# Performance work log

Measured on AMD Instinct MI355X. Metric: run time of the kernel, lower is better.

The kernel has to match this reference:

```python
import jax, jax.numpy as jnp
import numpy as np

# Sizes (see init_kwargs / shape_source)
N = 65536      # total points
B = 8          # batch elements
PPB = N // B   # points per batch element (8192, divisible by WS -> no padding)
D = 256        # d_model
H = 8          # nhead
DH = D // H
L = 4          # num_layers
FF = 2048      # torch TransformerEncoderLayer default dim_feedforward
RES = 128      # resolution (coordinate range / embedding table size)
BITS = 7       # ceil(log2(RES)); higher bits of morton loop are zero
WS = 128       # window_size
EPS = 1e-5     # LayerNorm eps


def setup_inputs() -> dict:
    key = jax.random.key(0)
    ks = jax.random.split(key, 16)
    s = 0.02
    batch_col = (jnp.arange(N) // PPB).astype(jnp.int32)
    xyz = jax.random.randint(ks[0], (N, 3), 0, RES, dtype=jnp.int32)
    coords = jnp.concatenate([batch_col[:, None], xyz], axis=1)
    features = jax.random.normal(ks[1], (N, D), jnp.float32)
    inp = {
        'coords': coords,
        'features': features,
        # learned positional embedding tables
        'pe_x': jax.random.normal(ks[2], (RES, D), jnp.float32) * s,
        'pe_y': jax.random.normal(ks[3], (RES, D), jnp.float32) * s,
        'pe_z': jax.random.normal(ks[4], (RES, D), jnp.float32) * s,
        'pe_s': jax.random.normal(ks[5], (RES, D), jnp.float32) * s,
        # stacked transformer encoder layer params (torch post-norm layer)
        'Wqkv': jax.random.normal(ks[6], (L, 3 * D, D), jnp.float32) * s,
        'bqkv': jnp.zeros((L, 3 * D), jnp.float32),
        'Wo': jax.random.normal(ks[7], (L, D, D), jnp.float32) * s,
        'bo': jnp.zeros((L, D), jnp.float32),
        'W1': jax.random.normal(ks[8], (L, FF, D), jnp.float32) * s,
        'b1': jnp.zeros((L, FF), jnp.float32),
        'W2': jax.random.normal(ks[9], (L, D, FF), jnp.float32) * s,
        'b2': jnp.zeros((L, D), jnp.float32),
        'g1': jnp.ones((L, D), jnp.float32),
        'be1': jnp.zeros((L, D), jnp.float32),
        'g2': jnp.ones((L, D), jnp.float32),
        'be2': jnp.zeros((L, D), jnp.float32),
    }
    return inp


def _morton_key(coords):
    # interleave bits of x,y,z (z lowest), prefix with batch index so batch order is preserved
    x, y, z = coords[:, 1], coords[:, 2], coords[:, 3]
    m = jnp.zeros_like(x)
    for i in range(BITS):
        m = m | (((x >> i) & 1) << (3 * i + 2)) \
              | (((y >> i) & 1) << (3 * i + 1)) \
              | (((z >> i) & 1) << (3 * i))
    return coords[:, 0] * (1 << (3 * BITS)) + m


def _ln(x, g, b):
    mu = jnp.mean(x, axis=-1, keepdims=True)
    var = jnp.mean(jnp.square(x - mu), axis=-1, keepdims=True)
    return (x - mu) * jax.lax.rsqrt(var + EPS) * g + b


def _encoder(x, params):
    # x: [Wn, WS, D]; torch TransformerEncoderLayer, post-norm, relu, no dropout (eval)
    scale = float(DH) ** -0.5

    def layer(h, p):
        Wqkv, bqkv, Wo, bo, W1, b1, W2, b2, g1, be1, g2, be2 = p
        Wn = h.shape[0]
        qkv = h @ Wqkv.T + bqkv                      # [Wn, WS, 3D]
        q, k, v = jnp.split(qkv, 3, axis=-1)
        q = q.reshape(Wn, WS, H, DH)
        k = k.reshape(Wn, WS, H, DH)
        v = v.reshape(Wn, WS, H, DH)
        att = jax.nn.softmax(jnp.einsum('wqhd,wkhd->whqk', q, k) * scale, axis=-1)
        o = jnp.einsum('whqk,wkhd->wqhd', att, v).reshape(Wn, WS, D) @ Wo.T + bo
        h = _ln(h + o, g1, be1)
        ff = jax.nn.relu(h @ W1.T + b1) @ W2.T + b2
        h = _ln(h + ff, g2, be2)
        return h, None

    x, _ = jax.lax.scan(layer, x, params)
    return x


def reference(coords, features, pe_x, pe_y, pe_z, pe_s,
              Wqkv, bqkv, Wo, bo, W1, b1, W2, b2, g1, be1, g2, be2):
    # 1) Morton sort (stable, batch-major)
    idx = jnp.argsort(_morton_key(coords))
    sc = coords[idx]
    sf = features[idx]
    # 2) learned positional encoding (stride = 1)
    pe = pe_x[sc[:, 1]] + pe_y[sc[:, 2]] + pe_z[sc[:, 3]] + pe_s[1]
    x = sf + pe
    # 3) window split: PPB % WS == 0, interval == 1 -> exact tiling, no padding
    x = x.reshape(-1, WS, D)                          # [Wn, WS, D]
    # 4) transformer encoder over windows
    x = _encoder(x, (Wqkv, bqkv, Wo, bo, W1, b1, W2, b2, g1, be1, g2, be2))
    # 5) gather back (all masks True -> simple reshape); output in sorted order
    return x.reshape(N, D)
```

## Files before the change

kernel.cpp:

```cpp
#include <hip/hip_runtime.h>

typedef unsigned int u32;
typedef unsigned short u16;

#define NPTS 65536
#define DMODEL 256
#define NHEAD 8
#define DHEAD 32
#define NLAYER 4
#define FFDIM 2048
#define WSIZE 128
#define LNEPS 1e-5f
#define RG 256

#define KSTR 36
#define VSTR 132
#define PSTR 132

typedef __attribute__((ext_vector_type(8))) short short8;
typedef __attribute__((ext_vector_type(4))) float floatx4;

__device__ __forceinline__ float bf2f(u16 v) {
    u32 u = ((u32)v) << 16;
    float f;
    __builtin_memcpy(&f, &u, 4);
    return f;
}
__device__ __forceinline__ u16 f2bf(float f) {
    u32 u;
    __builtin_memcpy(&u, &f, 4);
    u32 r = (u + 0x7fffu + ((u >> 16) & 1u)) >> 16;
    return (u16)r;
}

__device__ __forceinline__ void gl_lds16(const void* g, void* l) {
    __builtin_amdgcn_global_load_lds((const __attribute__((address_space(1))) u32*)g,
                                     (__attribute__((address_space(3))) u32*)l, 16, 0, 0);
}

__global__ __launch_bounds__(256) void morton_kernel(const int* __restrict__ coords,
                                                     u32* __restrict__ key, u32* __restrict__ val,
                                                     u32* __restrict__ ghist) {
    __shared__ u32 hh[256];
    int tid = threadIdx.x;
    hh[tid] = 0;
    int i = blockIdx.x * 256 + tid;
    int b = coords[4 * i + 0];
    int x = coords[4 * i + 1];
    int y = coords[4 * i + 2];
    int z = coords[4 * i + 3];
    u32 m = 0;
#pragma unroll
    for (int t = 0; t < 7; ++t) {
        m |= ((u32)((x >> t) & 1) << (3 * t + 2)) | ((u32)((y >> t) & 1) << (3 * t + 1)) |
             ((u32)((z >> t) & 1) << (3 * t));
    }
    u32 k = ((u32)b << 21) | m;
    key[i] = k;
    val[i] = (u32)i;
    __syncthreads();
    atomicAdd(&hh[k & 255u], 1u);
    __syncthreads();
    ghist[(size_t)tid * RG + blockIdx.x] = hh[tid];
}

__global__ __launch_bounds__(256) void hist_kernel(const u32* __restrict__ key, u32* __restrict__ ghist,
                                                   int shift) {
    __shared__ u32 h[256];
    int tid = threadIdx.x;
    h[tid] = 0;
    __syncthreads();
    u32 k = key[blockIdx.x * 256 + tid];
    atomicAdd(&h[(k >> shift) & 255u], 1u);
    __syncthreads();
    ghist[(size_t)tid * RG + blockIdx.x] = h[tid];
}

__global__ __launch_bounds__(256) void scan_up(u32* __restrict__ g, u32* __restrict__ aux) {
    __shared__ u32 wsum[4];
    int tid = threadIdx.x;
    int lane = tid & 63;
    int wave = tid >> 6;
    size_t base = (size_t)blockIdx.x * 1024 + (size_t)tid * 4;
    uint4 v = *(const uint4*)(g + base);
    u32 s = v.x + v.y + v.z + v.w;
    u32 inc = s;
#pragma unroll
    for (int off = 1; off < 64; off <<= 1) {
        u32 u = __shfl_up(inc, off, 64);
        if (lane >= off) inc += u;
    }
    if (lane == 63) wsum[wave] = inc;
    __syncthreads();
    u32 woff = 0;
    for (int w = 0; w < wave; ++w) woff += wsum[w];
    u32 excl = woff + inc - s;
    uint4 o;
    o.x = excl;
    o.y = excl + v.x;
    o.z = excl + v.x + v.y;
    o.w = excl + v.x + v.y + v.z;
    *(uint4*)(g + base) = o;
    if (tid == 255) aux[blockIdx.x] = woff + inc;
}

__global__ __launch_bounds__(256) void scatter_kernel(const u32* __restrict__ keyin, const u32* __restrict__ valin,
                                                      u32* __restrict__ keyout, u32* __restrict__ valout,
                                                      const u32* __restrict__ ghist, const u32* __restrict__ aux,
                                                      int shift) {
    __shared__ u32 whist[4][256];
    __shared__ u32 apre[64];
    int tid = threadIdx.x;
    int lane = tid & 63;
    int wave = tid >> 6;
    uint4 z = {0u, 0u, 0u, 0u};
    ((uint4*)&whist[0][0])[tid] = z;
    if (tid < 64) {
        u32 a = aux[tid];
        u32 inc = a;
#pragma unroll
        for (int off = 1; off < 64; off <<= 1) {
            u32 u = __shfl_up(inc, off, 64);
            if (lane >= off) inc += u;
        }
        apre[tid] = inc - a;
    }
    int gi = blockIdx.x * 256 + tid;
    u32 k = keyin[gi];
    u32 v = valin[gi];
    u32 b = (k >> shift) & 255u;
    __syncthreads();
    unsigned long long m = ~0ull;
#pragma unroll
    for (int bit = 0; bit < 8; ++bit) {
        unsigned long long bb = __ballot((int)((b >> bit) & 1u));
        m &= ((b >> bit) & 1u) ? bb : ~bb;
    }
    unsigned long long below = (lane == 0) ? 0ull : (m & ((1ull << lane) - 1ull));
    int rlane = __popcll(below);
    int cnt = __popcll(m);
    if (rlane == 0) whist[wave][b] = (u32)cnt;
    __syncthreads();
    u32 rank = (u32)rlane;
    for (int w = 0; w < wave; ++w) rank += whist[w][b];
    u32 e = b * (u32)RG + blockIdx.x;
    u32 dst = ghist[e] + apre[e >> 10] + rank;
    keyout[dst] = k;
    valout[dst] = v;
}

__global__ __launch_bounds__(256) void cvt_all_kernel(const float* __restrict__ s1, u16* __restrict__ d1, int n1,
                                                      const float* __restrict__ s2, u16* __restrict__ d2, int n2,
                                                      const float* __restrict__ s3, u16* __restrict__ d3, int n3,
                                                      const float* __restrict__ s4, u16* __restrict__ d4, int n4) {
    int i = blockIdx.x * 256 + threadIdx.x;
    if (i < n1) { d1[i] = f2bf(s1[i]); return; }
    i -= n1;
    if (i < n2) { d2[i] = f2bf(s2[i]); return; }
    i -= n2;
    if (i < n3) { d3[i] = f2bf(s3[i]); return; }
    i -= n3;
    if (i < n4) d4[i] = f2bf(s4[i]);
}

template <bool HF32>
__global__ __launch_bounds__(256) void gather_pe_kernel(const u32* __restrict__ idx, const int* __restrict__ coords,
                                                        const float* __restrict__ feat,
                                                        const float* __restrict__ pex, const float* __restrict__ pey,
                                                        const float* __restrict__ pez, const float* __restrict__ pes,
                                                        float* __restrict__ h, u16* __restrict__ xb) {
    int row = blockIdx.x * 4 + (threadIdx.x >> 6);
    int lane = threadIdx.x & 63;
    int src = (int)idx[row];
    int cx = coords[4 * src + 1];
    int cy = coords[4 * src + 2];
    int cz = coords[4 * src + 3];
    int c = lane * 4;
    float4 f = *(const float4*)(feat + (size_t)src * DMODEL + c);
    float4 px = *(const float4*)(pex + (size_t)cx * DMODEL + c);
    float4 py = *(const float4*)(pey + (size_t)cy * DMODEL + c);
    float4 pz = *(const float4*)(pez + (size_t)cz * DMODEL + c);
    float4 ps = *(const float4*)(pes + (size_t)1 * DMODEL + c);
    float4 r;
    r.x = f.x + px.x + py.x + pz.x + ps.x;
    r.y = f.y + px.y + py.y + pz.y + ps.y;
    r.z = f.z + px.z + py.z + pz.z + ps.z;
    r.w = f.w + px.w + py.w + pz.w + ps.w;
    if (HF32) *(float4*)(h + (size_t)row * DMODEL + c) = r;
    ushort4 o;
    o.x = f2bf(r.x);
    o.y = f2bf(r.y);
    o.z = f2bf(r.z);
    o.w = f2bf(r.w);
    *(ushort4*)(xb + (size_t)row * DMODEL + c) = o;
}

template <bool RELU, bool BF16OUT>
__global__ __launch_bounds__(256, 5) void gemm_bt(const u16* __restrict__ A, const u16* __restrict__ W,
                                                  const float* __restrict__ bias, void* __restrict__ Cout,
                                                  int M, int O, int K, size_t sz) {
    __shared__ __align__(16) u16 lA[2 * 128 * 32];
    __shared__ __align__(16) u16 lB[2 * 128 * 32];
    const int tid = threadIdx.x;
    const int lane = tid & 63;
    const int wave = tid >> 6;
    const int wr = wave >> 1;
    const int wc = wave & 1;
    const int quad = lane >> 4;
    const int l16 = lane & 15;
    const int kz = blockIdx.z;
    const int Kpart = K / (int)gridDim.z;
    const size_t row0 = (size_t)blockIdx.x * 128;
    const size_t col0 = (size_t)blockIdx.y * 128;
    floatx4 acc[4][4] = {};

    const int r0 = tid >> 2;
    const int sg0 = (tid & 3) ^ ((r0 >> 1) & 3);
    const u16* pA = A + (row0 + r0) * (size_t)K + (size_t)kz * Kpart + (sg0 << 3);
    const u16* pW = W + (col0 + r0) * (size_t)K + (size_t)kz * Kpart + (sg0 << 3);
    const size_t rstep = (size_t)64 * K;
    const int oA = tid * 8;

    const int nt = Kpart >> 5;
    gl_lds16(pA, lA + oA);
    gl_lds16(pA + rstep, lA + oA + 2048);
    gl_lds16(pW, lB + oA);
    gl_lds16(pW + rstep, lB + oA + 2048);
    pA += 32;
    pW += 32;

    const int sx = (quad ^ ((l16 >> 1) & 3)) << 3;
    const int rdA = (wr * 64 + l16) * 32 + sx;
    const int rdB = (wc * 64 + l16) * 32 + sx;
    int buf = 0;
    for (int t = 0; t < nt; ++t) {
        if (t + 1 < nt) {
            const int nb = (buf ^ 1) * 4096;
            gl_lds16(pA, lA + nb + oA);
            gl_lds16(pA + rstep, lA + nb + oA + 2048);
            gl_lds16(pW, lB + nb + oA);
            gl_lds16(pW + rstep, lB + nb + oA + 2048);
            pA += 32;
            pW += 32;
            asm volatile("s_waitcnt vmcnt(4)" ::: "memory");
        } else {
            asm volatile("s_waitcnt vmcnt(0)" ::: "memory");
        }
        __builtin_amdgcn_s_barrier();
        const u16* la = lA + buf * 4096 + rdA;
        const u16* lb = lB + buf * 4096 + rdB;
        short8 af[4], bf[4];
#pragma unroll
        for (int r = 0; r < 4; ++r) af[r] = *(const short8*)(la + r * 512);
#pragma unroll
        for (int c = 0; c < 4; ++c) bf[c] = *(const short8*)(lb + c * 512);
#pragma unroll
        for (int r = 0; r < 4; ++r)
#pragma unroll
            for (int c = 0; c < 4; ++c)
                acc[r][c] = __builtin_amdgcn_mfma_f32_16x16x32_bf16(af[r], bf[c], acc[r][c], 0, 0, 0);
        if (t + 1 < nt) __builtin_amdgcn_s_barrier();
        buf ^= 1;
    }

    float* Cf = (float*)Cout + (size_t)kz * sz;
#pragma unroll
    for (int r = 0; r < 4; ++r) {
#pragma unroll
        for (int c = 0; c < 4; ++c) {
            size_t col = col0 + wc * 64 + c * 16 + l16;
            float bv = (kz == 0) ? bias[col] : 0.f;
#pragma unroll
            for (int reg = 0; reg < 4; ++reg) {
                size_t row = row0 + wr * 64 + r * 16 + quad * 4 + reg;
                float v = acc[r][c][reg] + bv;
                if (RELU) v = fmaxf(v, 0.f);
                if (BF16OUT)
                    ((u16*)Cout)[row * O + col] = f2bf(v);
                else
                    Cf[row * O + col] = v;
            }
        }
    }
}

__global__ __launch_bounds__(256, 2) void gemm_w1(const u16* __restrict__ A, const u16* __restrict__ W,
                                                  const float* __restrict__ bias, u16* __restrict__ Cout,
                                                  int O, int K) {
    __shared__ __align__(16) u16 lA[2 * 128 * 32];
    __shared__ __align__(16) u16 lB[2 * 256 * 32];
    const int tid = threadIdx.x;
    const int lane = tid & 63;
    const int wave = tid >> 6;
    const int wr = wave >> 1;
    const int wc = wave & 1;
    const int quad = lane >> 4;
    const int l16 = lane & 15;
    const size_t row0 = (size_t)blockIdx.x * 128;
    const size_t col0 = (size_t)blockIdx.y * 256;
    floatx4 acc[4][8] = {};

    const int r0 = tid >> 2;
    const int sg0 = (tid & 3) ^ ((r0 >> 1) & 3);
    const u16* pA = A + (row0 + r0) * (size_t)K + (sg0 << 3);
    const u16* pW = W + (col0 + r0) * (size_t)K + (sg0 << 3);
    const size_t rstep = (size_t)64 * K;
    const int oA = tid * 8;

    const int nt = K >> 5;
    gl_lds16(pA, lA + oA);
    gl_lds16(pA + rstep, lA + oA + 2048);
    gl_lds16(pW, lB + oA);
    gl_lds16(pW + rstep, lB + oA + 2048);
    gl_lds16(pW + 2 * rstep, lB + oA + 4096);
    gl_lds16(pW + 3 * rstep, lB + oA + 6144);
    pA += 32;
    pW += 32;

    const int sx = (quad ^ ((l16 >> 1) & 3)) << 3;
    const int rdA = (wr * 64 + l16) * 32 + sx;
    const int rdB = (wc * 128 + l16) * 32 + sx;
    int buf = 0;
    for (int t = 0; t < nt; ++t) {
        if (t + 1 < nt) {
            const int na = (buf ^ 1) * 4096;
            const int nb = (buf ^ 1) * 8192;
            gl_lds16(pA, lA + na + oA);
            gl_lds16(pA + rstep, lA + na + oA + 2048);
            gl_lds16(pW, lB + nb + oA);
            gl_lds16(pW + rstep, lB + nb + oA + 2048);
            gl_lds16(pW + 2 * rstep, lB + nb + oA + 4096);
            gl_lds16(pW + 3 * rstep, lB + nb + oA + 6144);
            pA += 32;
            pW += 32;
            asm volatile("s_waitcnt vmcnt(6)" ::: "memory");
        } else {
            asm volatile("s_waitcnt vmcnt(0)" ::: "memory");
        }
        __builtin_amdgcn_s_barrier();
        const u16* la = lA + buf * 4096 + rdA;
        const u16* lb = lB + buf * 8192 + rdB;
        short8 af[4], bf[8];
#pragma unroll
        for (int r = 0; r < 4; ++r) af[r] = *(const short8*)(la + r * 512);
#pragma unroll
        for (int c = 0; c < 8; ++c) bf[c] = *(const short8*)(lb + c * 512);
#pragma unroll
        for (int r = 0; r < 4; ++r)
#pragma unroll
            for (int c = 0; c < 8; ++c)
                acc[r][c] = __builtin_amdgcn_mfma_f32_16x16x32_bf16(af[r], bf[c], acc[r][c], 0, 0, 0);
        if (t + 1 < nt) __builtin_amdgcn_s_barrier();
        buf ^= 1;
    }

#pragma unroll
    for (int r = 0; r < 4; ++r) {
#pragma unroll
        for (int c = 0; c < 8; ++c) {
            size_t col = col0 + wc * 128 + c * 16 + l16;
            float bv = bias[col];
#pragma unroll
            for (int reg = 0; reg < 4; ++reg) {
                size_t row = row0 + wr * 64 + r * 16 + quad * 4 + reg;
                float v = fmaxf(acc[r][c][reg] + bv, 0.f);
                Cout[row * O + col] = f2bf(v);
            }
        }
    }
}

__global__ __launch_bounds__(128) void attn_kernel(const u16* __restrict__ qkv, u16* __restrict__ outb) {
    const int wh = blockIdx.x;
    const int w = wh >> 3;
    const int h = wh & 7;
    const int tid = threadIdx.x;
    const int wave = tid >> 6;
    const int lane = tid & 63;
    const int quad = lane >> 4;
    const int l16 = lane & 15;
    __shared__ __align__(16) u16 lK[128 * KSTR];
    __shared__ __align__(16) u16 lVt[32 * VSTR];
    __shared__ __align__(16) u16 lP[128 * PSTR];
    const u16* base = qkv + (size_t)w * WSIZE * (3 * DMODEL);

    {
        const u16* krow = base + (size_t)tid * (3 * DMODEL) + DMODEL + h * DHEAD;
        const u16* vrow = base + (size_t)tid * (3 * DMODEL) + 2 * DMODEL + h * DHEAD;
#pragma unroll
        for (int p = 0; p < 4; ++p)
            *(short8*)&lK[tid * KSTR + p * 8] = *(const short8*)(krow + p * 8);
        u16 varr[32];
#pragma unroll
        for (int p = 0; p < 4; ++p)
            *(short8*)&varr[p * 8] = *(const short8*)(vrow + p * 8);
#pragma unroll
        for (int d = 0; d < DHEAD; ++d) lVt[d * VSTR + tid] = varr[d];
    }
    short8 af[4];
#pragma unroll
    for (int mi = 0; mi < 4; ++mi)
        af[mi] = *(const short8*)(base + (size_t)(wave * 64 + mi * 16 + l16) * (3 * DMODEL) + h * DHEAD + quad * 8);
    __syncthreads();

    floatx4 acc[4][8] = {};
#pragma unroll
    for (int ni = 0; ni < 8; ++ni) {
        short8 bk = *(const short8*)&lK[(ni * 16 + l16) * KSTR + quad * 8];
#pragma unroll
        for (int mi = 0; mi < 4; ++mi)
            acc[mi][ni] = __builtin_amdgcn_mfma_f32_16x16x32_bf16(af[mi], bk, acc[mi][ni], 0, 0, 0);
    }

    const float scale = 0.17677669529663687f;
    float inv[4][4];
#pragma unroll
    for (int mi = 0; mi < 4; ++mi) {
#pragma unroll
        for (int reg = 0; reg < 4; ++reg) {
            float m = acc[mi][0][reg];
#pragma unroll
            for (int ni = 1; ni < 8; ++ni) m = fmaxf(m, acc[mi][ni][reg]);
            m = fmaxf(m, __shfl_xor(m, 1, 64));
            m = fmaxf(m, __shfl_xor(m, 2, 64));
            m = fmaxf(m, __shfl_xor(m, 4, 64));
            m = fmaxf(m, __shfl_xor(m, 8, 64));
            float e[8];
            float sum = 0.f;
#pragma unroll
            for (int ni = 0; ni < 8; ++ni) {
                e[ni] = __expf((acc[mi][ni][reg] - m) * scale);
                sum += e[ni];
            }
            sum += __shfl_xor(sum, 1, 64);
            sum += __shfl_xor(sum, 2, 64);
            sum += __shfl_xor(sum, 4, 64);
            sum += __shfl_xor(sum, 8, 64);
            inv[mi][reg] = 1.f / sum;
            int row = wave * 64 + mi * 16 + quad * 4 + reg;
#pragma unroll
            for (int ni = 0; ni < 8; ++ni) lP[row * PSTR + ni * 16 + l16] = f2bf(e[ni]);
        }
    }

    floatx4 acc2[4][2] = {};
#pragma unroll
    for (int kt = 0; kt < 4; ++kt) {
        short8 pa[4];
#pragma unroll
        for (int mi = 0; mi < 4; ++mi)
            pa[mi] = *(const short8*)&lP[(wave * 64 + mi * 16 + l16) * PSTR + kt * 32 + quad * 8];
#pragma unroll
        for (int c = 0; c < 2; ++c) {
            short8 bv = *(const short8*)&lVt[(c * 16 + l16) * VSTR + kt * 32 + quad * 8];
#pragma unroll
            for (int mi = 0; mi < 4; ++mi)
                acc2[mi][c] = __builtin_amdgcn_mfma_f32_16x16x32_bf16(pa[mi], bv, acc2[mi][c], 0, 0, 0);
        }
    }

#pragma unroll
    for (int mi = 0; mi < 4; ++mi) {
#pragma unroll
        for (int c = 0; c < 2; ++c) {
#pragma unroll
            for (int reg = 0; reg < 4; ++reg) {
                int row = wave * 64 + mi * 16 + quad * 4 + reg;
                outb[(size_t)(w * WSIZE + row) * DMODEL + h * DHEAD + c * 16 + l16] =
                    f2bf(acc2[mi][c][reg] * inv[mi][reg]);
            }
        }
    }
}

template <bool HF32, bool OUTF32, int NS>
__global__ __launch_bounds__(256) void resid_ln_kernel(const void* __restrict__ hin, const float* __restrict__ delta,
                                                       const float* __restrict__ g, const float* __restrict__ b,
                                                       float* __restrict__ hout, void* __restrict__ nout,
                                                       size_t dstride) {
    int row = blockIdx.x * 4 + (threadIdx.x >> 6);
    int lane = threadIdx.x & 63;
    int c = lane * 4;
    float4 x;
    if (HF32) {
        x = *(const float4*)((const float*)hin + (size_t)row * DMODEL + c);
    } else {
        ushort4 hv = *(const ushort4*)((const u16*)hin + (size_t)row * DMODEL + c);
        x.x = bf2f(hv.x);
        x.y = bf2f(hv.y);
        x.z = bf2f(hv.z);
        x.w = bf2f(hv.w);
    }
    float4 d = *(const float4*)(delta + (size_t)row * DMODEL + c);
    if (NS == 2) {
        float4 d2 = *(const float4*)(delta + dstride + (size_t)row * DMODEL + c);
        d.x += d2.x;
        d.y += d2.y;
        d.z += d2.z;
        d.w += d2.w;
    }
    x.x += d.x;
    x.y += d.y;
    x.z += d.z;
    x.w += d.w;
    float s = x.x + x.y + x.z + x.w;
#pragma unroll
    for (int off = 32; off > 0; off >>= 1) s += __shfl_xor(s, off, 64);
    float mu = s * (1.f / 256.f);
    float d0 = x.x - mu, d1 = x.y - mu, d2 = x.z - mu, d3 = x.w - mu;
    float vs = d0 * d0 + d1 * d1 + d2 * d2 + d3 * d3;
#pragma unroll
    for (int off = 32; off > 0; off >>= 1) vs += __shfl_xor(vs, off, 64);
    float rs = rsqrtf(vs * (1.f / 256.f) + LNEPS);
    float4 gg = *(const float4*)(g + c);
    float4 bb = *(const float4*)(b + c);
    float4 y;
    y.x = d0 * rs * gg.x + bb.x;
    y.y = d1 * rs * gg.y + bb.y;
    y.z = d2 * rs * gg.z + bb.z;
    y.w = d3 * rs * gg.w + bb.w;
    if (HF32) *(float4*)(hout + (size_t)row * DMODEL + c) = y;
    if (OUTF32) {
        *(float4*)((float*)nout + (size_t)row * DMODEL + c) = y;
    } else {
        ushort4 o;
        o.x = f2bf(y.x);
        o.y = f2bf(y.y);
        o.z = f2bf(y.z);
        o.w = f2bf(y.w);
        *(ushort4*)((u16*)nout + (size_t)row * DMODEL + c) = o;
    }
}

extern "C" void kernel_launch(void* const* d_in, const int* in_sizes, int n_in,
                              void* d_out, int out_size, void* d_ws, size_t ws_size,
                              hipStream_t stream) {
    (void)in_sizes;
    (void)n_in;
    (void)out_size;
    const int* coords = (const int*)d_in[0];
    const float* feat = (const float*)d_in[1];
    const float* pex = (const float*)d_in[2];
    const float* pey = (const float*)d_in[3];
    const float* pez = (const float*)d_in[4];
    const float* pes = (const float*)d_in[5];
    const float* Wqkv = (const float*)d_in[6];
    const float* bqkv = (const float*)d_in[7];
    const float* Wo = (const float*)d_in[8];
    const float* bo = (const float*)d_in[9];
    const float* W1 = (const float*)d_in[10];
    const float* b1 = (const float*)d_in[11];
    const float* W2 = (const float*)d_in[12];
    const float* b2 = (const float*)d_in[13];
    const float* g1 = (const float*)d_in[14];
    const float* be1 = (const float*)d_in[15];
    const float* g2 = (const float*)d_in[16];
    const float* be2 = (const float*)d_in[17];

    auto al = [](size_t x) { return (x + 255) & ~(size_t)255; };
    const size_t sortB = 4 * al((size_t)NPTS * 4) + al((size_t)256 * RG * 4) + 256;
    const size_t wqkvB = al((size_t)NLAYER * 3 * DMODEL * DMODEL * 2);
    const size_t woB = al((size_t)NLAYER * DMODEL * DMODEL * 2);
    const size_t w1B = al((size_t)NLAYER * FFDIM * DMODEL * 2);
    const size_t w2B = al((size_t)NLAYER * DMODEL * FFDIM * 2);
    const size_t wB = wqkvB + woB + w1B + w2B;
    const size_t xbB = al((size_t)NPTS * DMODEL * 2);
    const size_t hB = al((size_t)NPTS * DMODEL * 4);

    int CH = 0, KSP = 1;
    bool modeA = true;
    for (int ch = 65536; ch >= 256 && !CH; ch >>= 1) {
        for (int ksp = 2; ksp >= 1; --ksp) {
            size_t need = sortB + wB + xbB + hB + al((size_t)ch * 2048) + al((size_t)ch * 1024 * ksp) + 65536;
            if (need <= ws_size) { CH = ch; KSP = ksp; modeA = true; break; }
        }
    }
    if (!CH) {
        for (int ch = 65536; ch >= 256 && !CH; ch >>= 1) {
            for (int ksp = 2; ksp >= 1; --ksp) {
                size_t need = sortB + wB + xbB + al((size_t)ch * 2048) + al((size_t)ch * 1024 * ksp) + 65536;
                if (need <= ws_size) { CH = ch; KSP = ksp; modeA = false; break; }
            }
        }
    }
    if (!CH) { CH = 256; KSP = 1; modeA = false; }

    char* ws = (char*)d_ws;
    size_t off = 0;
    auto alloc = [&](size_t bytes) -> void* {
        void* p = ws + off;
        off += al(bytes);
        return p;
    };
    u32* key0 = (u32*)alloc(NPTS * 4);
    u32* val0 = (u32*)alloc(NPTS * 4);
    u32* key1 = (u32*)alloc(NPTS * 4);
    u32* val1 = (u32*)alloc(NPTS * 4);
    u32* ghist = (u32*)alloc(256 * RG * 4);
    u32* aux = (u32*)alloc(64 * 4);
    u16* wqkv_b = (u16*)alloc((size_t)NLAYER * 3 * DMODEL * DMODEL * 2);
    u16* wo_b = (u16*)alloc((size_t)NLAYER * DMODEL * DMODEL * 2);
    u16* w1_b = (u16*)alloc((size_t)NLAYER * FFDIM * DMODEL * 2);
    u16* w2_b = (u16*)alloc((size_t)NLAYER * DMODEL * FFDIM * 2);
    u16* xb = (u16*)alloc((size_t)NPTS * DMODEL * 2);
    float* h = modeA ? (float*)alloc((size_t)NPTS * DMODEL * 4) : nullptr;
    u16* scratch1 = (u16*)alloc((size_t)CH * 2048);
    float* tmpc = (float*)alloc((size_t)CH * 1024 * KSP);
    const size_t dstride = (size_t)CH * DMODEL;

    morton_kernel<<<NPTS / 256, 256, 0, stream>>>(coords, key0, val0, ghist);

    u32 *ki = key0, *vi = val0, *ko = key1, *vo = val1;
    for (int p = 0; p < 3; ++p) {
        if (p > 0) hist_kernel<<<RG, 256, 0, stream>>>(ki, ghist, p * 8);
        scan_up<<<64, 256, 0, stream>>>(ghist, aux);
        scatter_kernel<<<RG, 256, 0, stream>>>(ki, vi, ko, vo, ghist, aux, p * 8);
        u32* t;
        t = ki; ki = ko; ko = t;
        t = vi; vi = vo; vo = t;
    }
    const u32* idx = vi;

    {
        const int n1 = NLAYER * 3 * DMODEL * DMODEL;
        const int n2 = NLAYER * DMODEL * DMODEL;
        const int n3 = NLAYER * FFDIM * DMODEL;
        const int n4 = NLAYER * DMODEL * FFDIM;
        cvt_all_kernel<<<(n1 + n2 + n3 + n4) / 256, 256, 0, stream>>>(Wqkv, wqkv_b, n1, Wo, wo_b, n2,
                                                                      W1, w1_b, n3, W2, w2_b, n4);
    }

    if (modeA)
        gather_pe_kernel<true><<<NPTS / 4, 256, 0, stream>>>(idx, coords, feat, pex, pey, pez, pes, h, xb);
    else
        gather_pe_kernel<false><<<NPTS / 4, 256, 0, stream>>>(idx, coords, feat, pex, pey, pez, pes, nullptr, xb);

    const int nch = NPTS / CH;
    u16* qkvc = scratch1;
    u16* attoutc = scratch1 + (size_t)CH * 768;
    u16* midc = scratch1;
    for (int l = 0; l < NLAYER; ++l) {
        for (int c = 0; c < nch; ++c) {
            u16* xc = xb + (size_t)c * CH * DMODEL;
            float* hc = modeA ? h + (size_t)c * CH * DMODEL : nullptr;
            gemm_bt<false, true><<<dim3(CH / 128, (3 * DMODEL) / 128), 256, 0, stream>>>(
                xc, wqkv_b + (size_t)l * 3 * DMODEL * DMODEL, bqkv + (size_t)l * 3 * DMODEL, qkvc,
                CH, 3 * DMODEL, DMODEL, 0);
            attn_kernel<<<(CH / WSIZE) * NHEAD, 128, 0, stream>>>(qkvc, attoutc);
            gemm_bt<false, false><<<dim3(CH / 128, DMODEL / 128), 256, 0, stream>>>(
                attoutc, wo_b + (size_t)l * DMODEL * DMODEL, bo + (size_t)l * DMODEL, tmpc,
                CH, DMODEL, DMODEL, 0);
            if (modeA)
                resid_ln_kernel<true, false, 1><<<CH / 4, 256, 0, stream>>>(hc, tmpc, g1 + (size_t)l * DMODEL,
                                                                            be1 + (size_t)l * DMODEL, hc, xc, dstride);
            else
                resid_ln_kernel<false, false, 1><<<CH / 4, 256, 0, stream>>>(xc, tmpc, g1 + (size_t)l * DMODEL,
                                                                             be1 + (size_t)l * DMODEL, nullptr, xc, dstride);
            const int MH = CH / 2;
            for (int hf = 0; hf < 2; ++hf) {
                const u16* xh = xc + (size_t)hf * MH * DMODEL;
                gemm_w1<<<dim3(MH / 128, FFDIM / 256), 256, 0, stream>>>(
                    xh, w1_b + (size_t)l * FFDIM * DMODEL, b1 + (size_t)l * FFDIM, midc, FFDIM, DMODEL);
                gemm_bt<false, false><<<dim3(MH / 128, DMODEL / 128, KSP), 256, 0, stream>>>(
                    midc, w2_b + (size_t)l * DMODEL * FFDIM, b2 + (size_t)l * DMODEL,
                    tmpc + (size_t)hf * MH * DMODEL, MH, DMODEL, FFDIM, dstride);
            }
            bool last = (l == NLAYER - 1);
            void* outc = last ? (void*)((float*)d_out + (size_t)c * CH * DMODEL) : (void*)xc;
            if (modeA) {
                if (last) {
                    if (KSP == 2)
                        resid_ln_kernel<true, true, 2><<<CH / 4, 256, 0, stream>>>(hc, tmpc, g2 + (size_t)l * DMODEL,
                                                                                   be2 + (size_t)l * DMODEL, hc, outc, dstride);
                    else
                        resid_ln_kernel<true, true, 1><<<CH / 4, 256, 0, stream>>>(hc, tmpc, g2 + (size_t)l * DMODEL,
                                                                                   be2 + (size_t)l * DMODEL, hc, outc, dstride);
                } else {
                    if (KSP == 2)
                        resid_ln_kernel<true, false, 2><<<CH / 4, 256, 0, stream>>>(hc, tmpc, g2 + (size_t)l * DMODEL,
                                                                                    be2 + (size_t)l * DMODEL, hc, outc, dstride);
                    else
                        resid_ln_kernel<true, false, 1><<<CH / 4, 256, 0, stream>>>(hc, tmpc, g2 + (size_t)l * DMODEL,
                                                                                    be2 + (size_t)l * DMODEL, hc, outc, dstride);
                }
            } else {
                if (last) {
                    if (KSP == 2)
                        resid_ln_kernel<false, true, 2><<<CH / 4, 256, 0, stream>>>(xc, tmpc, g2 + (size_t)l * DMODEL,
                                                                                    be2 + (size_t)l * DMODEL, nullptr, outc, dstride);
                    else
                        resid_ln_kernel<false, true, 1><<<CH / 4, 256, 0, stream>>>(xc, tmpc, g2 + (size_t)l * DMODEL,
                                                                                    be2 + (size_t)l * DMODEL, nullptr, outc, dstride);
                } else {
                    if (KSP == 2)
                        resid_ln_kernel<false, false, 2><<<CH / 4, 256, 0, stream>>>(xc, tmpc, g2 + (size_t)l * DMODEL,
                                                                                     be2 + (size_t)l * DMODEL, nullptr, outc, dstride);
                    else
                        resid_ln_kernel<false, false, 1><<<CH / 4, 256, 0, stream>>>(xc, tmpc, g2 + (size_t)l * DMODEL,
                                                                                     be2 + (size_t)l * DMODEL, nullptr, outc, dstride);
                }
            }
        }
    }
}
```

Before: 2.214 ms.

## Split FFN over hidden dimension with accumulating W2 GEMM instead of split-K

The FFN is now processed in two halves of the hidden dimension, each covering all chunk rows. The first W2 GEMM writes to the output buffer and the second adds into it, replacing the row-half split and the split-K second buffer. W2 is converted to bf16 in a relaid-out order so each 1024-wide K half is contiguous per output row. This drops the extra split-K partial buffer and its read in LayerNorm, which may let a larger chunk fit in the workspace. The cost is an fp32 read-modify-write of the output in the second GEMM.

```diff
diff --git a/kernel.cpp b/kernel.cpp
--- a/kernel.cpp
+++ b/kernel.cpp
@@ -160,7 +160,14 @@
     i -= n2;
     if (i < n3) { d3[i] = f2bf(s3[i]); return; }
     i -= n3;
-    if (i < n4) d4[i] = f2bf(s4[i]);
+    if (i < n4) {
+        int l = i >> 19;
+        int rem = i & 524287;
+        int o = rem >> 11;
+        int k = rem & 2047;
+        int out = (l << 19) + ((k >> 10) << 18) + (o << 10) + (k & 1023);
+        d4[out] = f2bf(s4[i]);
+    }
 }
 
 template <bool HF32>
@@ -195,10 +202,10 @@
     *(ushort4*)(xb + (size_t)row * DMODEL + c) = o;
 }
 
-template <bool RELU, bool BF16OUT>
+template <bool RELU, bool BF16OUT, bool ACCUM>
 __global__ __launch_bounds__(256, 5) void gemm_bt(const u16* __restrict__ A, const u16* __restrict__ W,
                                                   const float* __restrict__ bias, void* __restrict__ Cout,
-                                                  int M, int O, int K, size_t sz) {
+                                                  int M, int O, int K) {
     __shared__ __align__(16) u16 lA[2 * 128 * 32];
     __shared__ __align__(16) u16 lB[2 * 128 * 32];
     const int tid = threadIdx.x;
@@ -208,20 +215,18 @@
     const int wc = wave & 1;
     const int quad = lane >> 4;
     const int l16 = lane & 15;
-    const int kz = blockIdx.z;
-    const int Kpart = K / (int)gridDim.z;
     const size_t row0 = (size_t)blockIdx.x * 128;
     const size_t col0 = (size_t)blockIdx.y * 128;
     floatx4 acc[4][4] = {};
 
     const int r0 = tid >> 2;
     const int sg0 = (tid & 3) ^ ((r0 >> 1) & 3);
-    const u16* pA = A + (row0 + r0) * (size_t)K + (size_t)kz * Kpart + (sg0 << 3);
-    const u16* pW = W + (col0 + r0) * (size_t)K + (size_t)kz * Kpart + (sg0 << 3);
+    const u16* pA = A + (row0 + r0) * (size_t)K + (sg0 << 3);
+    const u16* pW = W + (col0 + r0) * (size_t)K + (sg0 << 3);
     const size_t rstep = (size_t)64 * K;
     const int oA = tid * 8;
 
-    const int nt = Kpart >> 5;
+    const int nt = K >> 5;
     gl_lds16(pA, lA + oA);
     gl_lds16(pA + rstep, lA + oA + 2048);
     gl_lds16(pW, lB + oA);
@@ -263,22 +268,24 @@
         buf ^= 1;
     }
 
-    float* Cf = (float*)Cout + (size_t)kz * sz;
 #pragma unroll
     for (int r = 0; r < 4; ++r) {
 #pragma unroll
         for (int c = 0; c < 4; ++c) {
             size_t col = col0 + wc * 64 + c * 16 + l16;
-            float bv = (kz == 0) ? bias[col] : 0.f;
+            float bv = bias ? bias[col] : 0.f;
 #pragma unroll
             for (int reg = 0; reg < 4; ++reg) {
                 size_t row = row0 + wr * 64 + r * 16 + quad * 4 + reg;
                 float v = acc[r][c][reg] + bv;
                 if (RELU) v = fmaxf(v, 0.f);
-                if (BF16OUT)
+                if (BF16OUT) {
                     ((u16*)Cout)[row * O + col] = f2bf(v);
-                else
-                    Cf[row * O + col] = v;
+                } else {
+                    float* p = (float*)Cout + row * O + col;
+                    if (ACCUM) v += *p;
+                    *p = v;
+                }
             }
         }
     }
@@ -473,11 +480,10 @@
     }
 }
 
-template <bool HF32, bool OUTF32, int NS>
+template <bool HF32, bool OUTF32>
 __global__ __launch_bounds__(256) void resid_ln_kernel(const void* __restrict__ hin, const float* __restrict__ delta,
                                                        const float* __restrict__ g, const float* __restrict__ b,
-                                                       float* __restrict__ hout, void* __restrict__ nout,
-                                                       size_t dstride) {
+                                                       float* __restrict__ hout, void* __restrict__ nout) {
     int row = blockIdx.x * 4 + (threadIdx.x >> 6);
     int lane = threadIdx.x & 63;
     int c = lane * 4;
@@ -492,13 +498,6 @@
         x.w = bf2f(hv.w);
     }
     float4 d = *(const float4*)(delta + (size_t)row * DMODEL + c);
-    if (NS == 2) {
-        float4 d2 = *(const float4*)(delta + dstride + (size_t)row * DMODEL + c);
-        d.x += d2.x;
-        d.y += d2.y;
-        d.z += d2.z;
-        d.w += d2.w;
-    }
     x.x += d.x;
     x.y += d.y;
     x.z += d.z;
@@ -567,23 +566,19 @@
     const size_t xbB = al((size_t)NPTS * DMODEL * 2);
     const size_t hB = al((size_t)NPTS * DMODEL * 4);
 
-    int CH = 0, KSP = 1;
+    int CH = 0;
     bool modeA = true;
     for (int ch = 65536; ch >= 256 && !CH; ch >>= 1) {
-        for (int ksp = 2; ksp >= 1; --ksp) {
-            size_t need = sortB + wB + xbB + hB + al((size_t)ch * 2048) + al((size_t)ch * 1024 * ksp) + 65536;
-            if (need <= ws_size) { CH = ch; KSP = ksp; modeA = true; break; }
-        }
+        size_t need = sortB + wB + xbB + hB + al((size_t)ch * 2048) + al((size_t)ch * 1024) + 65536;
+        if (need <= ws_size) { CH = ch; modeA = true; }
     }
     if (!CH) {
         for (int ch = 65536; ch >= 256 && !CH; ch >>= 1) {
-            for (int ksp = 2; ksp >= 1; --ksp) {
-                size_t need = sortB + wB + xbB + al((size_t)ch * 2048) + al((size_t)ch * 1024 * ksp) + 65536;
-                if (need <= ws_size) { CH = ch; KSP = ksp; modeA = false; break; }
-            }
-        }
-    }
-    if (!CH) { CH = 256; KSP = 1; modeA = false; }
+            size_t need = sortB + wB + xbB + al((size_t)ch * 2048) + al((size_t)ch * 1024) + 65536;
+            if (need <= ws_size) { CH = ch; modeA = false; }
+        }
+    }
+    if (!CH) { CH = 256; modeA = false; }
 
     char* ws = (char*)d_ws;
     size_t off = 0;
@@ -605,8 +600,7 @@
     u16* xb = (u16*)alloc((size_t)NPTS * DMODEL * 2);
     float* h = modeA ? (float*)alloc((size_t)NPTS * DMODEL * 4) : nullptr;
     u16* scratch1 = (u16*)alloc((size_t)CH * 2048);
-    float* tmpc = (float*)alloc((size_t)CH * 1024 * KSP);
-    const size_t dstride = (size_t)CH * DMODEL;
+    float* tmpc = (float*)alloc((size_t)CH * 1024);
 
     morton_kernel<<<NPTS / 256, 256, 0, stream>>>(coords, key0, val0, ghist);
 
@@ -643,62 +637,46 @@
         for (int c = 0; c < nch; ++c) {
             u16* xc = xb + (size_t)c * CH * DMODEL;
             float* hc = modeA ? h + (size_t)c * CH * DMODEL : nullptr;
-            gemm_bt<false, true><<<dim3(CH / 128, (3 * DMODEL) / 128), 256, 0, stream>>>(
+            gemm_bt<false, true, false><<<dim3(CH / 128, 6), 256, 0, stream>>>(
                 xc, wqkv_b + (size_t)l * 3 * DMODEL * DMODEL, bqkv + (size_t)l * 3 * DMODEL, qkvc,
-                CH, 3 * DMODEL, DMODEL, 0);
+                CH, 3 * DMODEL, DMODEL);
             attn_kernel<<<(CH / WSIZE) * NHEAD, 128, 0, stream>>>(qkvc, attoutc);
-            gemm_bt<false, false><<<dim3(CH / 128, DMODEL / 128), 256, 0, stream>>>(
+            gemm_bt<false, false, false><<<dim3(CH / 128, 2), 256, 0, stream>>>(
                 attoutc, wo_b + (size_t)l * DMODEL * DMODEL, bo + (size_t)l * DMODEL, tmpc,
-                CH, DMODEL, DMODEL, 0);
+                CH, DMODEL, DMODEL);
             if (modeA)
-                resid_ln_kernel<true, false, 1><<<CH / 4, 256, 0, stream>>>(hc, tmpc, g1 + (size_t)l * DMODEL,
-                                                                            be1 + (size_t)l * DMODEL, hc, xc, dstride);
+                resid_ln_kernel<true, false><<<CH / 4, 256, 0, stream>>>(hc, tmpc, g1 + (size_t)l * DMODEL,
+                                                                         be1 + (size_t)l * DMODEL, hc, xc);
             else
-                resid_ln_kernel<false, false, 1><<<CH / 4, 256, 0, stream>>>(xc, tmpc, g1 + (size_t)l * DMODEL,
-                                                                             be1 + (size_t)l * DMODEL, nullptr, xc, dstride);
-            const int MH = CH / 2;
-            for (int hf = 0; hf < 2; ++hf) {
-                const u16* xh = xc + (size_t)hf * MH * DMODEL;
-                gemm_w1<<<dim3(MH / 128, FFDIM / 256), 256, 0, stream>>>(
-                    xh, w1_b + (size_t)l * FFDIM * DMODEL, b1 + (size_t)l * FFDIM, midc, FFDIM, DMODEL);
-                gemm_bt<false, false><<<dim3(MH / 128, DMODEL / 128, KSP), 256, 0, stream>>>(
-                    midc, w2_b + (size_t)l * DMODEL * FFDIM, b2 + (size_t)l * DMODEL,
-                    tmpc + (size_t)hf * MH * DMODEL, MH, DMODEL, FFDIM, dstride);
+                resid_ln_kernel<false, false><<<CH / 4, 256, 0, stream>>>(xc, tmpc, g1 + (size_t)l * DMODEL,
+                                                                          be1 + (size_t)l * DMODEL, nullptr, xc);
+            for (int j = 0; j < 2; ++j) {
+                gemm_w1<<<dim3(CH / 128, 4), 256, 0, stream>>>(
+                    xc, w1_b + (size_t)l * FFDIM * DMODEL + (size_t)j * 1024 * DMODEL,
+                    b1 + (size_t)l * FFDIM + j * 1024, midc, 1024, DMODEL);
+                if (j == 0)
+                    gemm_bt<false, false, false><<<dim3(CH / 128, 2), 256, 0, stream>>>(
+                        midc, w2_b + (size_t)l * 524288, b2 + (size_t)l * DMODEL, tmpc, CH, DMODEL, 1024);
+                else
+                    gemm_bt<false, false, true><<<dim3(CH / 128, 2), 256, 0, stream>>>(
+                        midc, w2_b + (size_t)l * 524288 + 262144, nullptr, tmpc, CH, DMODEL, 1024);
             }
             bool last = (l == NLAYER - 1);
             void* outc = last ? (void*)((float*)d_out + (size_t)c * CH * DMODEL) : (void*)xc;
             if (modeA) {
-                if (last) {
-                    if (KSP == 2)
-                        resid_ln_kernel<true, true, 2><<<CH / 4, 256, 0, stream>>>(hc, tmpc, g2 + (size_t)l * DMODEL,
-                                                                                   be2 + (size_t)l * DMODEL, hc, outc, dstride);
-                    else
-                        resid_ln_kernel<true, true, 1><<<CH / 4, 256, 0, stream>>>(hc, tmpc, g2 + (size_t)l * DMODEL,
-                                                                                   be2 + (size_t)l * DMODEL, hc, outc, dstride);
-                } else {
-                    if (KSP == 2)
-                        resid_ln_kernel<true, false, 2><<<CH / 4, 256, 0, stream>>>(hc, tmpc, g2 + (size_t)l * DMODEL,
-                                                                                    be2 + (size_t)l * DMODEL, hc, outc, dstride);
-                    else
-                        resid_ln_kernel<true, false, 1><<<CH / 4, 256, 0, stream>>>(hc, tmpc, g2 + (size_t)l * DMODEL,
-                                                                                    be2 + (size_t)l * DMODEL, hc, outc, dstride);
-                }
+                if (last)
+                    resid_ln_kernel<true, true><<<CH / 4, 256, 0, stream>>>(hc, tmpc, g2 + (size_t)l * DMODEL,
+                                                                            be2 + (size_t)l * DMODEL, hc, outc);
+                else
+                    resid_ln_kernel<true, false><<<CH / 4, 256, 0, stream>>>(hc, tmpc, g2 + (size_t)l * DMODEL,
+                                                                             be2 + (size_t)l * DMODEL, hc, outc);
             } else {
-                if (last) {
-                    if (KSP == 2)
-                        resid_ln_kernel<false, true, 2><<<CH / 4, 256, 0, stream>>>(xc, tmpc, g2 + (size_t)l * DMODEL,
-                                                                                    be2 + (size_t)l * DMODEL, nullptr, outc, dstride);
-                    else
-                        resid_ln_kernel<false, true, 1><<<CH / 4, 256, 0, stream>>>(xc, tmpc, g2 + (size_t)l * DMODEL,
-                                                                                    be2 + (size_t)l * DMODEL, nullptr, outc, dstride);
-                } else {
-                    if (KSP == 2)
-                        resid_ln_kernel<false, false, 2><<<CH / 4, 256, 0, stream>>>(xc, tmpc, g2 + (size_t)l * DMODEL,
-                                                                                     be2 + (size_t)l * DMODEL, nullptr, outc, dstride);
-                    else
-                        resid_ln_kernel<false, false, 1><<<CH / 4, 256, 0, stream>>>(xc, tmpc, g2 + (size_t)l * DMODEL,
-                                                                                     be2 + (size_t)l * DMODEL, nullptr, outc, dstride);
-                }
+                if (last)
+                    resid_ln_kernel<false, true><<<CH / 4, 256, 0, stream>>>(xc, tmpc, g2 + (size_t)l * DMODEL,
+                                                                             be2 + (size_t)l * DMODEL, nullptr, outc);
+                else
+                    resid_ln_kernel<false, false><<<CH / 4, 256, 0, stream>>>(xc, tmpc, g2 + (size_t)l * DMODEL,
+                                                                              be2 + (size_t)l * DMODEL, nullptr, outc);
             }
         }
     }
```

Result: slower. 2.280 ms (+3.0%).
